# Performance work log

Measured on AMD Instinct MI355X. Metric: run time of the kernel, lower is better.

## Reference

```python
import jax, jax.numpy as jnp
from jax import lax
import numpy as np

STRIDE = 2
PADDING = 2
DILATION = 1
K = 5


def _maxpool3d(y, k):
    # NCDHW, kernel=stride=k, VALID padding (matches nn.MaxPool3d(kernel_size=k))
    return lax.reduce_window(y, -jnp.inf, lax.max,
                             (1, 1, k, k, k), (1, 1, k, k, k), 'VALID')


def setup_inputs() -> dict:
    key = jax.random.key(0)
    k1, k2, k3 = jax.random.split(key, 3)
    x = jax.random.normal(k1, (16, 32, 48, 48, 48), dtype=jnp.float32)
    # ConvTranspose3d weight layout: (C_in, C_out, Kd, Kh, Kw)
    weight = jax.random.normal(k2, (32, 64, 5, 5, 5), dtype=jnp.float32) * 0.02
    bias = jax.random.normal(k3, (64,), dtype=jnp.float32) * 0.02
    return {"x": x, "weight": weight, "bias": bias}


def reference(x, weight, bias):
    # Fold the post-conv channel sum into the weights: sum over C_out (dim 1)
    cw = weight.sum(axis=1)            # (C_in, Kd, Kh, Kw)
    cb = bias.sum()                    # scalar combined bias
    # Transposed conv == conv with lhs_dilation=stride, spatially flipped kernel,
    # and padding = dilation*(k-1) - padding on each side.
    pad = DILATION * (K - 1) - PADDING  # = 2
    kernel = jnp.flip(cw, axis=(1, 2, 3))[None]  # (1, C_in, Kd, Kh, Kw) OIDHW
    out = lax.conv_general_dilated(
        x, kernel,
        window_strides=(1, 1, 1),
        padding=[(pad, pad)] * 3,
        lhs_dilation=(STRIDE, STRIDE, STRIDE),
        rhs_dilation=(DILATION, DILATION, DILATION),
        dimension_numbers=('NCDHW', 'OIDHW', 'NCDHW'))
    out = out + cb                      # (N, 1, 95, 95, 95)
    out = _maxpool3d(out, 2)            # (N, 1, 47, 47, 47)
    out = _maxpool3d(out, 3)            # (N, 1, 15, 15, 15)
    return jnp.sum(out, axis=1, keepdims=True)  # no-op sum over single channel
```

## Files before the change

kernel.cpp:

```cpp
#include <hip/hip_runtime.h>
#include <math.h>


#define XS (48*48*48)

typedef __fp16 h2 __attribute__((ext_vector_type(2)));
union UH { unsigned u; h2 h; };

__device__ __forceinline__ unsigned pk16(float a, float b) {
    UH r; r.h = __builtin_amdgcn_cvt_pkrtz(a, b);
    return r.u;
}

__global__ void fold_kernel(const float* __restrict__ w,
                            const float* __restrict__ bias,
                            unsigned* __restrict__ ws) {
    int t = blockIdx.x * blockDim.x + threadIdx.x;
    if (t < 2000) {
        int pix = t >> 4, sc = t & 15;
        int kd = pix / 25, r25 = pix % 25;
        int kh = r25 / 5,  kw = r25 % 5;
        int chunk = sc >> 3, lc = sc & 7;
        int cg = lc >> 1,    sub = lc & 1;
        const float* p0 = w + (size_t)(2 * sc) * 64 * 125 + pix;
        const float* p1 = p0 + 64 * 125;
        float s0 = 0.f, s1 = 0.f;
        #pragma unroll 8
        for (int o = 0; o < 64; ++o) { s0 += p0[o * 125]; s1 += p1[o * 125]; }
        ws[(((kd * 2 + chunk) * 4 + cg) * 52) + (kh * 5 + kw) * 2 + sub] = pk16(s0, s1);
    } else if (t < 2080) {
        int i = t - 2000;
        ws[(i >> 1) * 52 + 50 + (i & 1)] = 0;
    } else if (t == 2080) {
        float s = 0.f;
        for (int o = 0; o < 64; ++o) s += bias[o];
        ((float*)ws)[2080] = s;
    }
}

__global__ __launch_bounds__(128)
void fused_kernel(const float* __restrict__ x,
                  const unsigned* __restrict__ wsrc,
                  float* __restrict__ out) {
    __shared__ unsigned xt[4 * 425 * 2];
    __shared__ unsigned cwS[2080];
    __shared__ float red[30];

    const int tid = threadIdx.x;
    int bid = ((blockIdx.x & 7) * 1350) + (blockIdx.x >> 3);
    const int bw = bid % 3;  bid /= 3;
    const int jh = bid % 15; bid /= 15;
    const int jd = bid % 15; const int n = bid / 15;
    const int d0 = 3 * jd - 1, h0 = 3 * jh - 1, w0 = 15 * bw - 1;

    for (int e = tid; e < 520; e += 128)
        ((uint4*)cwS)[e] = ((const uint4*)wsrc)[e];

    const int fo = tid / 24;
    const int r  = tid % 24;
    const int rd = r >> 2;
    const int cg = r & 3;
    const bool active = tid < 120;

    const int ntd  = (rd & 1) ? 2 : 3;
    const int kd0  = rd & 1;
    const int lid0 = (rd + 4 - kd0) >> 1;

    float acc[36];
    #pragma unroll
    for (int i = 0; i < 36; ++i) acc[i] = 0.f;

    const int c2  = tid & 7;
    const int p00 = tid >> 3;
    const int wgrp = c2 >> 1, wsub = c2 & 1;

    for (int chunk = 0; chunk < 2; ++chunk) {
        __syncthreads();
        {
            const float* xc0 = x + ((size_t)n * 32 + chunk * 16 + 2 * c2) * XS;
            const float* xc1 = xc0 + XS;
            for (int p = p00; p < 425; p += 16) {
                int dz = p / 85;
                int rm = p - dz * 85;
                int dy = rm / 17;
                int dx = rm - dy * 17;
                int gd = d0 + dz, gh = h0 + dy, gw = w0 + dx;
                unsigned v = 0;
                if (((unsigned)gd < 48u) & ((unsigned)gh < 48u) & ((unsigned)gw < 48u)) {
                    int off = (gd * 48 + gh) * 48 + gw;
                    v = pk16(xc0[off], xc1[off]);
                }
                xt[wgrp * 850 + p * 2 + wsub] = v;
            }
        }
        __syncthreads();

        if (active) {
            #pragma unroll
            for (int a = 0; a < 3; ++a) {
                if (a < ntd) {
                    const int lid = lid0 - a;
                    const int kd  = kd0 + 2 * a;

                    union { uint4 q[13]; uint2 d[26]; } W;
                    {
                        const uint4* wb = (const uint4*)&cwS[((kd * 2 + chunk) * 4 + cg) * 52];
                        #pragma unroll
                        for (int i = 0; i < 13; ++i) W.q[i] = wb[i];
                    }

                    const unsigned* xb = &xt[cg * 850 + (lid * 85 + 3 * fo) * 2];

                    #pragma unroll
                    for (int lih = 0; lih < 5; ++lih) {
                        uint2 ir[5];
                        #pragma unroll
                        for (int iw = 0; iw < 5; ++iw)
                            ir[iw] = *(const uint2*)&xb[(lih * 17 + iw) * 2];
                        #pragma unroll
                        for (int kh = 0; kh < 5; ++kh) {
                            const int rh = 2 * lih + kh - 4;
                            if (rh >= 0 && rh < 6) {
                                #pragma unroll
                                for (int liw = 0; liw < 5; ++liw) {
                                    #pragma unroll
                                    for (int kw = 0; kw < 5; ++kw) {
                                        const int rw = 2 * liw + kw - 4;
                                        if (rw >= 0 && rw < 6) {
                                            UH x0, x1, w0v, w1v;
                                            x0.u = ir[liw].x;
                                            x1.u = ir[liw].y;
                                            w0v.u = W.d[kh * 5 + kw].x;
                                            w1v.u = W.d[kh * 5 + kw].y;
                                            float s = acc[rh * 6 + rw];
                                            s = __builtin_amdgcn_fdot2(x0.h, w0v.h, s, false);
                                            s = __builtin_amdgcn_fdot2(x1.h, w1v.h, s, false);
                                            acc[rh * 6 + rw] = s;
                                        }
                                    }
                                }
                            }
                        }
                    }
                }
            }
        }
    }

    if (active) {
        #pragma unroll
        for (int i = 0; i < 36; ++i) {
            acc[i] += __shfl_xor(acc[i], 1);
            acc[i] += __shfl_xor(acc[i], 2);
        }
        if (cg == 0) {
            float m = -INFINITY;
            #pragma unroll
            for (int i = 0; i < 36; ++i) m = fmaxf(m, acc[i]);
            red[fo * 6 + rd] = m;
        }
    }
    __syncthreads();
    if (tid < 5) {
        float m = -INFINITY;
        #pragma unroll
        for (int k = 0; k < 6; ++k) m = fmaxf(m, red[tid * 6 + k]);
        float cb = ((const float*)wsrc)[2080];
        out[(((size_t)n * 15 + jd) * 15 + jh) * 15 + 5 * bw + tid] = m + cb;
    }
}

extern "C" void kernel_launch(void* const* d_in, const int* in_sizes, int n_in,
                              void* d_out, int out_size, void* d_ws, size_t ws_size,
                              hipStream_t stream) {
    const float* x = (const float*)d_in[0];
    const float* w = (const float*)d_in[1];
    const float* b = (const float*)d_in[2];
    float* out = (float*)d_out;
    unsigned* ws = (unsigned*)d_ws;

    fold_kernel<<<9, 256, 0, stream>>>(w, b, ws);

    fused_kernel<<<3 * 15 * 15 * 16, 128, 0, stream>>>(x, ws, out);
}
```

Before: 260.6 us.

## Process two batch samples per block with wave-uniform depth parity

Each block now has 256 threads and handles two batch samples, so the folded weight table is loaded into shared memory once per two output tiles. Threads are remapped so that each 64-lane wave has a single depth parity, making the ntd/kd loop bounds uniform within the wave instead of divergent. An empty asm barrier pins the weight registers to stop the compiler from rematerialising shared loads. The cost is double the shared-memory tile size per block, which may lower occupancy, and wasted lanes (4 of 64 per wave).

```diff
diff --git a/kernel.cpp b/kernel.cpp
--- a/kernel.cpp
+++ b/kernel.cpp
@@ -38,47 +38,52 @@
     }
 }
 
-__global__ __launch_bounds__(128)
+union WU { uint4 q; uint2 d[2]; unsigned u[4]; };
+
+__global__ __launch_bounds__(256)
 void fused_kernel(const float* __restrict__ x,
                   const unsigned* __restrict__ wsrc,
                   float* __restrict__ out) {
-    __shared__ unsigned xt[4 * 425 * 2];
+    __shared__ unsigned xt[2 * 4 * 425 * 2];
     __shared__ unsigned cwS[2080];
-    __shared__ float red[30];
+    __shared__ float red[60];
 
     const int tid = threadIdx.x;
-    int bid = ((blockIdx.x & 7) * 1350) + (blockIdx.x >> 3);
+    int bid = ((blockIdx.x & 7) * 675) + (blockIdx.x >> 3);
     const int bw = bid % 3;  bid /= 3;
     const int jh = bid % 15; bid /= 15;
-    const int jd = bid % 15; const int n = bid / 15;
+    const int jd = bid % 15; const int nb = bid / 15;
     const int d0 = 3 * jd - 1, h0 = 3 * jh - 1, w0 = 15 * bw - 1;
 
-    for (int e = tid; e < 520; e += 128)
+    const int t    = tid >> 7;
+    const int n    = nb * 2 + t;
+
+    for (int e = tid; e < 520; e += 256)
         ((uint4*)cwS)[e] = ((const uint4*)wsrc)[e];
 
-    const int fo = tid / 24;
-    const int r  = tid % 24;
-    const int rd = r >> 2;
-    const int cg = r & 3;
-    const bool active = tid < 120;
+    const int lane = tid & 63;
+    const int wpar = (tid >> 6) & 1;
+    const int fo   = lane / 12;
+    const int rdi  = (lane % 12) >> 2;
+    const int cg   = lane & 3;
+    const bool active = lane < 60;
+    const int rd   = 2 * rdi + wpar;
+    const int ntd  = wpar ? 2 : 3;
 
-    const int ntd  = (rd & 1) ? 2 : 3;
-    const int kd0  = rd & 1;
-    const int lid0 = (rd + 4 - kd0) >> 1;
+    const int tid2 = tid & 127;
+    const int c2   = tid2 & 7;
+    const int p00  = tid2 >> 3;
 
     float acc[36];
     #pragma unroll
     for (int i = 0; i < 36; ++i) acc[i] = 0.f;
-
-    const int c2  = tid & 7;
-    const int p00 = tid >> 3;
-    const int wgrp = c2 >> 1, wsub = c2 & 1;
 
     for (int chunk = 0; chunk < 2; ++chunk) {
         __syncthreads();
         {
             const float* xc0 = x + ((size_t)n * 32 + chunk * 16 + 2 * c2) * XS;
             const float* xc1 = xc0 + XS;
+            unsigned* xdst = &xt[t * 3400 + (c2 >> 1) * 850 + (c2 & 1)];
             for (int p = p00; p < 425; p += 16) {
                 int dz = p / 85;
                 int rm = p - dz * 85;
@@ -90,7 +95,7 @@
                     int off = (gd * 48 + gh) * 48 + gw;
                     v = pk16(xc0[off], xc1[off]);
                 }
-                xt[wgrp * 850 + p * 2 + wsub] = v;
+                xdst[p * 2] = v;
             }
         }
         __syncthreads();
@@ -99,17 +104,21 @@
             #pragma unroll
             for (int a = 0; a < 3; ++a) {
                 if (a < ntd) {
-                    const int lid = lid0 - a;
-                    const int kd  = kd0 + 2 * a;
+                    const int lid = rdi + 2 - a;
+                    const int kd  = wpar + 2 * a;
 
-                    union { uint4 q[13]; uint2 d[26]; } W;
+                    WU W[13];
                     {
                         const uint4* wb = (const uint4*)&cwS[((kd * 2 + chunk) * 4 + cg) * 52];
                         #pragma unroll
-                        for (int i = 0; i < 13; ++i) W.q[i] = wb[i];
+                        for (int i = 0; i < 13; ++i) {
+                            W[i].q = wb[i];
+                            asm volatile("" : "+v"(W[i].q.x), "+v"(W[i].q.y),
+                                              "+v"(W[i].q.z), "+v"(W[i].q.w));
+                        }
                     }
 
-                    const unsigned* xb = &xt[cg * 850 + (lid * 85 + 3 * fo) * 2];
+                    const unsigned* xb = &xt[t * 3400 + cg * 850 + (lid * 85 + 3 * fo) * 2];
 
                     #pragma unroll
                     for (int lih = 0; lih < 5; ++lih) {
@@ -127,11 +136,12 @@
                                     for (int kw = 0; kw < 5; ++kw) {
                                         const int rw = 2 * liw + kw - 4;
                                         if (rw >= 0 && rw < 6) {
+                                            const int j2 = (kh * 5 + kw) * 2;
                                             UH x0, x1, w0v, w1v;
-                                            x0.u = ir[liw].x;
-                                            x1.u = ir[liw].y;
-                                            w0v.u = W.d[kh * 5 + kw].x;
-                                            w1v.u = W.d[kh * 5 + kw].y;
+                                            x0.u  = ir[liw].x;
+                                            x1.u  = ir[liw].y;
+                                            w0v.u = W[j2 >> 2].u[j2 & 3];
+                                            w1v.u = W[(j2 + 1) >> 2].u[(j2 + 1) & 3];
                                             float s = acc[rh * 6 + rw];
                                             s = __builtin_amdgcn_fdot2(x0.h, w0v.h, s, false);
                                             s = __builtin_amdgcn_fdot2(x1.h, w1v.h, s, false);
@@ -157,16 +167,17 @@
             float m = -INFINITY;
             #pragma unroll
             for (int i = 0; i < 36; ++i) m = fmaxf(m, acc[i]);
-            red[fo * 6 + rd] = m;
+            red[t * 30 + fo * 6 + rd] = m;
         }
     }
     __syncthreads();
-    if (tid < 5) {
+    if (tid < 10) {
+        const int tt = tid / 5, ff = tid % 5;
         float m = -INFINITY;
         #pragma unroll
-        for (int k = 0; k < 6; ++k) m = fmaxf(m, red[tid * 6 + k]);
+        for (int k = 0; k < 6; ++k) m = fmaxf(m, red[tt * 30 + ff * 6 + k]);
         float cb = ((const float*)wsrc)[2080];
-        out[(((size_t)n * 15 + jd) * 15 + jh) * 15 + 5 * bw + tid] = m + cb;
+        out[(((size_t)(nb * 2 + tt) * 15 + jd) * 15 + jh) * 15 + 5 * bw + ff] = m + cb;
     }
 }
 
@@ -181,5 +192,5 @@
 
     fold_kernel<<<9, 256, 0, stream>>>(w, b, ws);
 
-    fused_kernel<<<3 * 15 * 15 * 16, 128, 0, stream>>>(x, ws, out);
+    fused_kernel<<<3 * 15 * 15 * 8, 256, 0, stream>>>(x, ws, out);
 }
```

Measured after the change: 236.3 us. 1.1x faster.
